# Kernel tuning notes

Measured on AMD Instinct MI355X. Metric: run time of the kernel, lower is better.

The kernel has to match this reference:

```python
import jax, jax.numpy as jnp
import numpy as np

T_LEN = 1024
N_IN = 512
BATCH = 32
SURR_ALPHA = 4.0  # slope of the sigmoid surrogate gradient


@jax.custom_vjp
def heaviside_sg(x):
    # spike = Heaviside(x); backward uses sigmoid surrogate derivative
    return (x >= 0).astype(x.dtype)

def _hs_fwd(x):
    return heaviside_sg(x), x

def _hs_bwd(x, g):
    s = jax.nn.sigmoid(SURR_ALPHA * x)
    return (g * SURR_ALPHA * s * (1.0 - s),)

heaviside_sg.defvjp(_hs_fwd, _hs_bwd)


def setup_inputs() -> dict:
    key = jax.random.key(0)
    k1, k2, k3 = jax.random.split(key, 3)
    current = jax.random.normal(k1, (T_LEN, BATCH, N_IN), dtype=jnp.float32)
    beta = jax.random.uniform(k2, (N_IN,), dtype=jnp.float32)  # per-channel decay in (0,1)
    v_init = jax.random.normal(k3, (BATCH, N_IN), dtype=jnp.float32)
    v_th = jnp.ones((T_LEN, BATCH, N_IN), dtype=jnp.float32)
    return {"current": current, "beta": beta, "v_init": v_init, "v_th": v_th}


def reference(current, beta, v_init, v_th):
    # Torch version: grouped causal conv1d with kernel beta^{T-1-k}, i.e.
    # membrane[t] = sum_{j<=t} beta^{t-j} * current[j], with current[0] += beta*v_init.
    # Equivalent O(T) linear recurrence: m_t = beta*m_{t-1} + c_t, m_{-1}=v_init.
    def step(m, c):
        m = beta * m + c  # beta (N,) broadcasts over (B,N)
        return m, m

    m_last, membrane = jax.lax.scan(step, v_init, current)  # membrane: (T,B,N)

    # surrogate-gradient spike function
    spikes = heaviside_sg(membrane - v_th)  # (T,B,N)

    # triangular phi kernel: z[t] = sum_{j<=t} (t-j+1)*spikes[j] == double cumsum
    z = jnp.cumsum(jnp.cumsum(spikes, axis=0), axis=0)  # (T,B,N)

    # Block.g: keep entries equal to 1, zero everything else; gradient is identity
    # (the subtracted term is detached in the torch code).
    gz = z - jax.lax.stop_gradient(jnp.where(z == 1.0, 0.0, z))

    return gz, z, m_last  # m_last == membrane[:, :, -1] in torch layout (B,N)
```

## Files before the change

### kernel.cpp

```cpp
#include <hip/hip_runtime.h>


#define T_LEN 1024
#define N_IN  512
#define BN    16384
#define U     16

struct Buf { float c[U]; float v[U]; };

__device__ __forceinline__ void prefetch(Buf& b, const float* __restrict__ cp,
                                         const float* __restrict__ vp, int t0) {
    const float* __restrict__ c = cp + (size_t)t0 * BN;
    const float* __restrict__ v = vp + (size_t)t0 * BN;
#pragma unroll
    for (int u = 0; u < U; ++u) {
        b.c[u] = c[(size_t)u * BN];
        b.v[u] = v[(size_t)u * BN];
    }
}

__device__ __forceinline__ unsigned process16(const Buf& b, float beta, float& m) {
    unsigned mask = 0u;
#pragma unroll
    for (int u = 0; u < U; ++u) {
        m = fmaf(beta, m, b.c[u]);
        mask |= (m >= b.v[u]) ? (1u << u) : 0u;
    }
    return mask;
}

__global__ __launch_bounds__(512, 2) void snn_scan(
        const float* __restrict__ cur, const float* __restrict__ beta,
        const float* __restrict__ vini, const float* __restrict__ vth,
        float* __restrict__ gz, float* __restrict__ zo, float* __restrict__ ml)
{
    __shared__ unsigned bits[T_LEN / 32][64];

    const int lane = threadIdx.x & 63;
    const int wave = threadIdx.x >> 6;
    const int i = blockIdx.x * 64 + lane;

    if (wave == 0) {
        const float bta = beta[i & (N_IN - 1)];
        float m = vini[i];
        const float* cp = cur + i;
        const float* vp = vth + i;

        Buf b0, b1, b2, b3;
        prefetch(b0, cp, vp, 0);
        prefetch(b1, cp, vp, U);
        prefetch(b2, cp, vp, 2 * U);
        prefetch(b3, cp, vp, 3 * U);

        for (int t0 = 0; t0 < T_LEN; t0 += 4 * U) {
            unsigned m0 = process16(b0, bta, m);
            if (t0 + 4 * U < T_LEN) prefetch(b0, cp, vp, t0 + 4 * U);
            unsigned m1 = process16(b1, bta, m);
            if (t0 + 5 * U < T_LEN) prefetch(b1, cp, vp, t0 + 5 * U);
            bits[t0 >> 5][lane] = m0 | (m1 << 16);
            unsigned m2 = process16(b2, bta, m);
            if (t0 + 6 * U < T_LEN) prefetch(b2, cp, vp, t0 + 6 * U);
            unsigned m3 = process16(b3, bta, m);
            if (t0 + 7 * U < T_LEN) prefetch(b3, cp, vp, t0 + 7 * U);
            bits[(t0 >> 5) + 1][lane] = m2 | (m3 << 16);
        }
        ml[i] = m;
    }
    __syncthreads();

    int C = 0;
    int Z = 0;
    const int d0 = wave * 4;
    for (int d = 0; d < d0; ++d) {
        unsigned u = bits[d][lane];
#pragma unroll
        for (int b = 0; b < 32; ++b) {
            C += (u >> b) & 1u;
            Z += C;
        }
    }

    float* __restrict__ gp = gz + (size_t)(d0 * 32) * BN + i;
    float* __restrict__ zp = zo + (size_t)(d0 * 32) * BN + i;
    for (int d = 0; d < 4; ++d) {
        unsigned u = bits[d0 + d][lane];
#pragma unroll
        for (int b = 0; b < 32; ++b) {
            C += (u >> b) & 1u;
            Z += C;
            const size_t off = (size_t)(d * 32 + b) * BN;
            gp[off] = (Z == 1) ? 1.0f : 0.0f;
            zp[off] = (float)Z;
        }
    }
}

extern "C" void kernel_launch(void* const* d_in, const int* in_sizes, int n_in,
                              void* d_out, int out_size, void* d_ws, size_t ws_size,
                              hipStream_t stream) {
    const float* cur  = (const float*)d_in[0];
    const float* beta = (const float*)d_in[1];
    const float* vini = (const float*)d_in[2];
    const float* vth  = (const float*)d_in[3];
    float* gz = (float*)d_out;
    float* zo = gz + (size_t)T_LEN * BN;
    float* ml = zo + (size_t)T_LEN * BN;
    snn_scan<<<BN / 64, 512, 0, stream>>>(cur, beta, vini, vth, gz, zo, ml);
}
```

Before: 247.1 us.

## Pipeline scan and cumsum writeback in chunks with vectorized float4 stores

Splits the time axis into chunks of 128 steps. Wave 0 computes spike bits for chunk k while the other seven waves do the double-cumsum and write outputs for chunk k-1, with a block barrier after each chunk. The writeback is reorganized so each lane owns 4 channels and stores float4 rows, and 4-row groups are distributed round-robin across the seven consumer waves. This overlaps the serial recurrence with output stores and removes the redundant prefix recomputation each wave did before, at the cost of nine block barriers and every consumer wave scanning every chunk in full.

```diff
diff --git a/kernel.cpp b/kernel.cpp
--- a/kernel.cpp
+++ b/kernel.cpp
@@ -5,11 +5,14 @@
 #define N_IN  512
 #define BN    16384
 #define U     16
+#define CT    128
+#define NC    (T_LEN / CT)
 
 struct Buf { float c[U]; float v[U]; };
 
 __device__ __forceinline__ void prefetch(Buf& b, const float* __restrict__ cp,
                                          const float* __restrict__ vp, int t0) {
+    if (t0 >= T_LEN) return;
     const float* __restrict__ c = cp + (size_t)t0 * BN;
     const float* __restrict__ v = vp + (size_t)t0 * BN;
 #pragma unroll
@@ -36,62 +39,92 @@
 {
     __shared__ unsigned bits[T_LEN / 32][64];
 
-    const int lane = threadIdx.x & 63;
-    const int wave = threadIdx.x >> 6;
-    const int i = blockIdx.x * 64 + lane;
+    const int lane   = threadIdx.x & 63;
+    const int wave   = threadIdx.x >> 6;
+    const int chbase = blockIdx.x * 64;
 
+    float bta = 0.0f, m = 0.0f;
+    const float* cp = nullptr;
+    const float* vp = nullptr;
+    Buf b0, b1, b2, b3;
     if (wave == 0) {
-        const float bta = beta[i & (N_IN - 1)];
-        float m = vini[i];
-        const float* cp = cur + i;
-        const float* vp = vth + i;
-
-        Buf b0, b1, b2, b3;
+        const int i = chbase + lane;
+        bta = beta[i & (N_IN - 1)];
+        m   = vini[i];
+        cp  = cur + i;
+        vp  = vth + i;
         prefetch(b0, cp, vp, 0);
         prefetch(b1, cp, vp, U);
         prefetch(b2, cp, vp, 2 * U);
         prefetch(b3, cp, vp, 3 * U);
-
-        for (int t0 = 0; t0 < T_LEN; t0 += 4 * U) {
-            unsigned m0 = process16(b0, bta, m);
-            if (t0 + 4 * U < T_LEN) prefetch(b0, cp, vp, t0 + 4 * U);
-            unsigned m1 = process16(b1, bta, m);
-            if (t0 + 5 * U < T_LEN) prefetch(b1, cp, vp, t0 + 5 * U);
-            bits[t0 >> 5][lane] = m0 | (m1 << 16);
-            unsigned m2 = process16(b2, bta, m);
-            if (t0 + 6 * U < T_LEN) prefetch(b2, cp, vp, t0 + 6 * U);
-            unsigned m3 = process16(b3, bta, m);
-            if (t0 + 7 * U < T_LEN) prefetch(b3, cp, vp, t0 + 7 * U);
-            bits[(t0 >> 5) + 1][lane] = m2 | (m3 << 16);
-        }
-        ml[i] = m;
-    }
-    __syncthreads();
-
-    int C = 0;
-    int Z = 0;
-    const int d0 = wave * 4;
-    for (int d = 0; d < d0; ++d) {
-        unsigned u = bits[d][lane];
-#pragma unroll
-        for (int b = 0; b < 32; ++b) {
-            C += (u >> b) & 1u;
-            Z += C;
-        }
     }
 
-    float* __restrict__ gp = gz + (size_t)(d0 * 32) * BN + i;
-    float* __restrict__ zp = zo + (size_t)(d0 * 32) * BN + i;
-    for (int d = 0; d < 4; ++d) {
-        unsigned u = bits[d0 + d][lane];
+    const int row_sub = lane >> 4;
+    const int chgrp   = lane & 15;
+    const int wsel    = wave - 1;
+    int C0 = 0, C1 = 0, C2 = 0, C3 = 0;
+    int Z0 = 0, Z1 = 0, Z2 = 0, Z3 = 0;
+    float* __restrict__ gbase = gz + chbase + 4 * chgrp;
+    float* __restrict__ zbase = zo + chbase + 4 * chgrp;
+
+    for (int cc = 0; cc <= NC; ++cc) {
+        if (wave == 0) {
+            if (cc < NC) {
+                const int t0 = cc * CT;
+                unsigned ma, mb;
+                ma = process16(b0, bta, m); prefetch(b0, cp, vp, t0 + 4 * U);
+                mb = process16(b1, bta, m); prefetch(b1, cp, vp, t0 + 5 * U);
+                bits[(t0 >> 5) + 0][lane] = ma | (mb << 16);
+                ma = process16(b2, bta, m); prefetch(b2, cp, vp, t0 + 6 * U);
+                mb = process16(b3, bta, m); prefetch(b3, cp, vp, t0 + 7 * U);
+                bits[(t0 >> 5) + 1][lane] = ma | (mb << 16);
+                ma = process16(b0, bta, m); prefetch(b0, cp, vp, t0 + 8 * U);
+                mb = process16(b1, bta, m); prefetch(b1, cp, vp, t0 + 9 * U);
+                bits[(t0 >> 5) + 2][lane] = ma | (mb << 16);
+                ma = process16(b2, bta, m); prefetch(b2, cp, vp, t0 + 10 * U);
+                mb = process16(b3, bta, m); prefetch(b3, cp, vp, t0 + 11 * U);
+                bits[(t0 >> 5) + 3][lane] = ma | (mb << 16);
+                if (cc == NC - 1) ml[chbase + lane] = m;
+            }
+        } else if (cc >= 1) {
+            const int pc = cc - 1;
+            int qm = (pc * 32) % 7;
 #pragma unroll
-        for (int b = 0; b < 32; ++b) {
-            C += (u >> b) & 1u;
-            Z += C;
-            const size_t off = (size_t)(d * 32 + b) * BN;
-            gp[off] = (Z == 1) ? 1.0f : 0.0f;
-            zp[off] = (float)Z;
+            for (int d = 0; d < 4; ++d) {
+                const uint4 u = *reinterpret_cast<const uint4*>(
+                                    &bits[4 * pc + d][4 * chgrp]);
+#pragma unroll
+                for (int sub = 0; sub < 8; ++sub) {
+                    int zq0 = 0, zq1 = 0, zq2 = 0, zq3 = 0;
+#pragma unroll
+                    for (int r = 0; r < 4; ++r) {
+                        const int bp = sub * 4 + r;
+                        C0 += (int)((u.x >> bp) & 1u); Z0 += C0;
+                        C1 += (int)((u.y >> bp) & 1u); Z1 += C1;
+                        C2 += (int)((u.z >> bp) & 1u); Z2 += C2;
+                        C3 += (int)((u.w >> bp) & 1u); Z3 += C3;
+                        zq0 = (row_sub == r) ? Z0 : zq0;
+                        zq1 = (row_sub == r) ? Z1 : zq1;
+                        zq2 = (row_sub == r) ? Z2 : zq2;
+                        zq3 = (row_sub == r) ? Z3 : zq3;
+                    }
+                    if (qm == wsel) {
+                        const int q = pc * 32 + d * 8 + sub;
+                        const size_t roff = (size_t)(q * 4 + row_sub) * BN;
+                        float4 zf = make_float4((float)zq0, (float)zq1,
+                                                (float)zq2, (float)zq3);
+                        float4 gf = make_float4(zq0 == 1 ? 1.0f : 0.0f,
+                                                zq1 == 1 ? 1.0f : 0.0f,
+                                                zq2 == 1 ? 1.0f : 0.0f,
+                                                zq3 == 1 ? 1.0f : 0.0f);
+                        *reinterpret_cast<float4*>(gbase + roff) = gf;
+                        *reinterpret_cast<float4*>(zbase + roff) = zf;
+                    }
+                    qm = (qm == 6) ? 0 : qm + 1;
+                }
+            }
         }
+        __syncthreads();
     }
 }
 
```

New measurement: 322.4 us. 30.4% more time.

## Split scan and expansion into two kernels with workspace prefix carries

Applied to the files above, without the earlier changes.

The fused kernel is split in two. The first does the serial membrane scan per channel and writes spike bitmasks plus packed running count and cumulative-sum prefixes for each 32-step word into workspace. The second kernel is launched over all time-words and channel groups, rebuilds z from those prefixes and writes gz and z with float4 stores. This exposes far more parallelism for the large output writes, which were previously done by only 8 waves per 64 channels. The cost is an extra launch, a workspace round trip, and a dependence on the workspace size; the old fused kernel is kept as a fallback. The packed prefix uses 11 bits for C and 21 bits for Z, which could overflow if Z exceeds about 2 million, though with T=1024 Z stays below about 525k.

```diff
diff --git a/kernel.cpp b/kernel.cpp
--- a/kernel.cpp
+++ b/kernel.cpp
@@ -5,11 +5,13 @@
 #define N_IN  512
 #define BN    16384
 #define U     16
+#define DW    (T_LEN / 32)
 
 struct Buf { float c[U]; float v[U]; };
 
 __device__ __forceinline__ void prefetch(Buf& b, const float* __restrict__ cp,
                                          const float* __restrict__ vp, int t0) {
+    if (t0 >= T_LEN) return;
     const float* __restrict__ c = cp + (size_t)t0 * BN;
     const float* __restrict__ v = vp + (size_t)t0 * BN;
 #pragma unroll
@@ -19,17 +21,102 @@
     }
 }
 
-__device__ __forceinline__ unsigned process16(const Buf& b, float beta, float& m) {
+__device__ __forceinline__ unsigned process16(const Buf& b, float beta, float& m,
+                                              int& C, int& Z) {
     unsigned mask = 0u;
 #pragma unroll
     for (int u = 0; u < U; ++u) {
         m = fmaf(beta, m, b.c[u]);
-        mask |= (m >= b.v[u]) ? (1u << u) : 0u;
+        const int s = (m >= b.v[u]) ? 1 : 0;
+        mask |= (unsigned)s << u;
+        C += s;
+        Z += C;
     }
     return mask;
 }
 
-__global__ __launch_bounds__(512, 2) void snn_scan(
+
+__global__ __launch_bounds__(64, 1) void snn_scan(
+        const float* __restrict__ cur, const float* __restrict__ beta,
+        const float* __restrict__ vini, const float* __restrict__ vth,
+        unsigned* __restrict__ bitsg, unsigned* __restrict__ Pc,
+        float* __restrict__ ml)
+{
+    const int i = blockIdx.x * 64 + threadIdx.x;
+    const float bta = beta[i & (N_IN - 1)];
+    float m = vini[i];
+    int C = 0, Z = 0;
+
+    const float* cp = cur + i;
+    const float* vp = vth + i;
+
+    Buf b0, b1, b2, b3;
+    prefetch(b0, cp, vp, 0);
+    prefetch(b1, cp, vp, U);
+    prefetch(b2, cp, vp, 2 * U);
+    prefetch(b3, cp, vp, 3 * U);
+
+    for (int t0 = 0; t0 < T_LEN; t0 += 4 * U) {
+        const int d = t0 >> 5;
+        Pc[(size_t)d * BN + i] = (unsigned)C | ((unsigned)Z << 11);
+        unsigned ma = process16(b0, bta, m, C, Z);   prefetch(b0, cp, vp, t0 + 4 * U);
+        unsigned mb = process16(b1, bta, m, C, Z);   prefetch(b1, cp, vp, t0 + 5 * U);
+        bitsg[(size_t)d * BN + i] = ma | (mb << 16);
+        Pc[(size_t)(d + 1) * BN + i] = (unsigned)C | ((unsigned)Z << 11);
+        ma = process16(b2, bta, m, C, Z);            prefetch(b2, cp, vp, t0 + 6 * U);
+        mb = process16(b3, bta, m, C, Z);            prefetch(b3, cp, vp, t0 + 7 * U);
+        bitsg[(size_t)(d + 1) * BN + i] = ma | (mb << 16);
+    }
+    ml[i] = m;
+}
+
+__global__ __launch_bounds__(256, 4) void snn_expand(
+        const unsigned* __restrict__ bitsg, const unsigned* __restrict__ Pc,
+        float* __restrict__ gz, float* __restrict__ zo)
+{
+    const int d  = blockIdx.x & (DW - 1);
+    const int cb = blockIdx.x / DW;
+    const int cg = threadIdx.x & 63;
+    const int tt = threadIdx.x >> 6;
+    const int ch = cb * 256 + cg * 4;
+
+    const uint4 u  = *reinterpret_cast<const uint4*>(&bitsg[(size_t)d * BN + ch]);
+    const uint4 p4 = *reinterpret_cast<const uint4*>(&Pc[(size_t)d * BN + ch]);
+    int C0 = (int)(p4.x & 0x7FFu), Z0 = (int)(p4.x >> 11);
+    int C1 = (int)(p4.y & 0x7FFu), Z1 = (int)(p4.y >> 11);
+    int C2 = (int)(p4.z & 0x7FFu), Z2 = (int)(p4.z >> 11);
+    int C3 = (int)(p4.w & 0x7FFu), Z3 = (int)(p4.w >> 11);
+
+    const int pre = tt * 8;
+    for (int b = 0; b < pre; ++b) {
+        C0 += (int)((u.x >> b) & 1u); Z0 += C0;
+        C1 += (int)((u.y >> b) & 1u); Z1 += C1;
+        C2 += (int)((u.z >> b) & 1u); Z2 += C2;
+        C3 += (int)((u.w >> b) & 1u); Z3 += C3;
+    }
+
+    float* __restrict__ gp = gz + (size_t)(d * 32 + pre) * BN + ch;
+    float* __restrict__ zp = zo + (size_t)(d * 32 + pre) * BN + ch;
+#pragma unroll
+    for (int r = 0; r < 8; ++r) {
+        const int b = pre + r;
+        C0 += (int)((u.x >> b) & 1u); Z0 += C0;
+        C1 += (int)((u.y >> b) & 1u); Z1 += C1;
+        C2 += (int)((u.z >> b) & 1u); Z2 += C2;
+        C3 += (int)((u.w >> b) & 1u); Z3 += C3;
+        const float4 gf = make_float4(Z0 == 1 ? 1.0f : 0.0f,
+                                      Z1 == 1 ? 1.0f : 0.0f,
+                                      Z2 == 1 ? 1.0f : 0.0f,
+                                      Z3 == 1 ? 1.0f : 0.0f);
+        const float4 zf = make_float4((float)Z0, (float)Z1,
+                                      (float)Z2, (float)Z3);
+        *reinterpret_cast<float4*>(gp + (size_t)r * BN) = gf;
+        *reinterpret_cast<float4*>(zp + (size_t)r * BN) = zf;
+    }
+}
+
+
+__global__ __launch_bounds__(512, 2) void snn_fused(
         const float* __restrict__ cur, const float* __restrict__ beta,
         const float* __restrict__ vini, const float* __restrict__ vth,
         float* __restrict__ gz, float* __restrict__ zo, float* __restrict__ ml)
@@ -43,6 +130,7 @@
     if (wave == 0) {
         const float bta = beta[i & (N_IN - 1)];
         float m = vini[i];
+        int Cd = 0, Zd = 0;
         const float* cp = cur + i;
         const float* vp = vth + i;
 
@@ -53,31 +141,27 @@
         prefetch(b3, cp, vp, 3 * U);
 
         for (int t0 = 0; t0 < T_LEN; t0 += 4 * U) {
-            unsigned m0 = process16(b0, bta, m);
-            if (t0 + 4 * U < T_LEN) prefetch(b0, cp, vp, t0 + 4 * U);
-            unsigned m1 = process16(b1, bta, m);
-            if (t0 + 5 * U < T_LEN) prefetch(b1, cp, vp, t0 + 5 * U);
+            unsigned m0 = process16(b0, bta, m, Cd, Zd);
+            prefetch(b0, cp, vp, t0 + 4 * U);
+            unsigned m1 = process16(b1, bta, m, Cd, Zd);
+            prefetch(b1, cp, vp, t0 + 5 * U);
             bits[t0 >> 5][lane] = m0 | (m1 << 16);
-            unsigned m2 = process16(b2, bta, m);
-            if (t0 + 6 * U < T_LEN) prefetch(b2, cp, vp, t0 + 6 * U);
-            unsigned m3 = process16(b3, bta, m);
-            if (t0 + 7 * U < T_LEN) prefetch(b3, cp, vp, t0 + 7 * U);
+            unsigned m2 = process16(b2, bta, m, Cd, Zd);
+            prefetch(b2, cp, vp, t0 + 6 * U);
+            unsigned m3 = process16(b3, bta, m, Cd, Zd);
+            prefetch(b3, cp, vp, t0 + 7 * U);
             bits[(t0 >> 5) + 1][lane] = m2 | (m3 << 16);
         }
         ml[i] = m;
     }
     __syncthreads();
 
-    int C = 0;
-    int Z = 0;
+    int C = 0, Z = 0;
     const int d0 = wave * 4;
     for (int d = 0; d < d0; ++d) {
         unsigned u = bits[d][lane];
 #pragma unroll
-        for (int b = 0; b < 32; ++b) {
-            C += (u >> b) & 1u;
-            Z += C;
-        }
+        for (int b = 0; b < 32; ++b) { C += (u >> b) & 1u; Z += C; }
     }
 
     float* __restrict__ gp = gz + (size_t)(d0 * 32) * BN + i;
@@ -105,5 +189,15 @@
     float* gz = (float*)d_out;
     float* zo = gz + (size_t)T_LEN * BN;
     float* ml = zo + (size_t)T_LEN * BN;
-    snn_scan<<<BN / 64, 512, 0, stream>>>(cur, beta, vini, vth, gz, zo, ml);
-}
+
+    const size_t need = (size_t)DW * BN * sizeof(unsigned) * 2;
+
+    if (d_ws != nullptr && ws_size >= need) {
+        unsigned* bitsg = (unsigned*)d_ws;
+        unsigned* Pc = bitsg + (size_t)DW * BN;
+        snn_scan<<<BN / 64, 64, 0, stream>>>(cur, beta, vini, vth, bitsg, Pc, ml);
+        snn_expand<<<DW * (BN / 256), 256, 0, stream>>>(bitsg, Pc, gz, zo);
+    } else {
+        snn_fused<<<BN / 64, 512, 0, stream>>>(cur, beta, vini, vth, gz, zo, ml);
+    }
+}
```

Measured after the change: 252.9 us. 1.02x slower.
